# Optimization experiments

Hardware: AMD Instinct MI355X
Metric: run time of the kernel (lower is better)

## Reference

```python
import jax, jax.numpy as jnp
import numpy as np
from jax import lax

EPS = 1e-8

def squash(x, axis=-1):
    # s = (|x|^2 / (1+|x|^2)) * x / |x|, norm over `axis`
    sq = jnp.sum(x * x, axis=axis, keepdims=True)
    return (sq / (1.0 + sq)) * x / jnp.sqrt(sq + EPS)

def _conv(x, w, b, stride):
    y = lax.conv_general_dilated(x, w, window_strides=(stride, stride), padding='VALID',
                                 dimension_numbers=('NCHW', 'OIHW', 'NCHW'))
    return y + b[None, :, None, None]

def setup_inputs() -> dict:
    key = jax.random.key(0)
    ks = jax.random.split(key, 12)
    B = 256
    return {
        'x': jax.random.uniform(ks[0], (B, 1, 28, 28), jnp.float32),
        'conv1_w': jax.random.normal(ks[1], (256, 1, 9, 9), jnp.float32) * 0.1,
        'conv1_b': jax.random.normal(ks[2], (256,), jnp.float32) * 0.01,
        'conv2_w': jax.random.normal(ks[3], (256, 256, 9, 9), jnp.float32) * 0.02,
        'conv2_b': jax.random.normal(ks[4], (256,), jnp.float32) * 0.01,
        'W': jax.random.normal(ks[5], (10, 1152, 8, 16), jnp.float32) * 0.05,
        'dec_w1': jax.random.normal(ks[6], (160, 512), jnp.float32) * 0.05,
        'dec_b1': jnp.zeros((512,), jnp.float32),
        'dec_w2': jax.random.normal(ks[7], (512, 1024), jnp.float32) * 0.04,
        'dec_b2': jnp.zeros((1024,), jnp.float32),
        'dec_w3': jax.random.normal(ks[8], (1024, 784), jnp.float32) * 0.03,
        'dec_b3': jnp.zeros((784,), jnp.float32),
    }

def reference(x, conv1_w, conv1_b, conv2_w, conv2_b, W, dec_w1, dec_b1, dec_w2, dec_b2, dec_w3, dec_b3):
    B = x.shape[0]
    h = jax.nn.relu(_conv(x, conv1_w, conv1_b, 1))          # [B,256,20,20]
    h = jax.nn.relu(_conv(h, conv2_w, conv2_b, 2))          # [B,256,6,6]
    u = squash(h.reshape(B, 1152, 8))                       # [B,1152,8]
    # u_hat[b,c,n,f] = sum_d u[b,n,d] * W[c,n,d,f]
    u_hat = jnp.einsum('bnd,cndf->bcnf', u, W)              # [B,10,1152,16]
    # dynamic routing, 3 iterations; softmax over the 1152 input-capsule axis
    # (faithful to original: softmax dim=2, b constant along the 16 axis)
    b_logits = jnp.zeros((B, 10, 1152), u_hat.dtype)
    v = None
    for i in range(3):
        c = jax.nn.softmax(b_logits, axis=2)                # [B,10,1152]
        s = jnp.einsum('bcn,bcnf->bcf', c, u_hat)           # [B,10,16]
        v = squash(s)
        if i != 2:
            b_logits = b_logits + jnp.einsum('bcf,bcnf->bcn', v, u_hat)
    class_probs = jnp.sqrt(jnp.sum(v * v, axis=-1) + EPS)   # [B,10]
    idx = jnp.argmax(class_probs, axis=-1)
    mask = jax.nn.one_hot(idx, 10, dtype=v.dtype)           # [B,10]
    r = (v * mask[:, :, None]).reshape(B, 160)
    r = jax.nn.relu(r @ dec_w1 + dec_b1)
    r = jax.nn.relu(r @ dec_w2 + dec_b2)
    recons = jax.nn.sigmoid(r @ dec_w3 + dec_b3)            # [B,784]
    return (class_probs, recons)
```

## Files before the change

### kernel.cpp

```cpp
#include <hip/hip_runtime.h>
#include <hip/hip_bf16.h>
#include <math.h>

typedef _Float16 f16;
typedef f16 f16x8 __attribute__((ext_vector_type(8)));
typedef f16 f16x4 __attribute__((ext_vector_type(4)));
typedef float f32x16 __attribute__((ext_vector_type(16)));


__global__ __launch_bounds__(256) void conv1_kernel(
    const float* __restrict__ x, const float* __restrict__ w,
    const float* __restrict__ bias, f16* __restrict__ outh,
    float* __restrict__ outf, int mode)
{
    const int b = blockIdx.y;
    const int cg = blockIdx.x;
    const int t = threadIdx.x;

    __shared__ float xs[784];
    __shared__ float wt[81 * 16];
    __shared__ float bs[16];

    for (int i = t; i < 784; i += 256) xs[i] = x[b * 784 + i];
    for (int i = t; i < 1296; i += 256) {
        int k = i >> 4, cc = i & 15;
        wt[i] = w[(cg * 16 + cc) * 81 + k];
    }
    if (t < 16) bs[t] = bias[cg * 16 + t];
    __syncthreads();

    if (t >= 200) return;
    const int pos = t * 2;
    const int oy = pos / 20, ox = pos % 20;
    float4 A0[4], A1[4];
    #pragma unroll
    for (int g = 0; g < 4; ++g) { A0[g] = make_float4(0,0,0,0); A1[g] = make_float4(0,0,0,0); }

    for (int ky = 0; ky < 9; ++ky) {
        const float* xr = &xs[(oy + ky) * 28 + ox];
        #pragma unroll
        for (int kx = 0; kx < 9; ++kx) {
            float x0 = xr[kx], x1 = xr[kx + 1];
            const float4* wp = (const float4*)&wt[(ky * 9 + kx) << 4];
            #pragma unroll
            for (int g = 0; g < 4; ++g) {
                float4 wv = wp[g];
                A0[g].x = fmaf(x0, wv.x, A0[g].x); A0[g].y = fmaf(x0, wv.y, A0[g].y);
                A0[g].z = fmaf(x0, wv.z, A0[g].z); A0[g].w = fmaf(x0, wv.w, A0[g].w);
                A1[g].x = fmaf(x1, wv.x, A1[g].x); A1[g].y = fmaf(x1, wv.y, A1[g].y);
                A1[g].z = fmaf(x1, wv.z, A1[g].z); A1[g].w = fmaf(x1, wv.w, A1[g].w);
            }
        }
    }

    float va[16], vb[16];
    #pragma unroll
    for (int g = 0; g < 4; ++g) {
        va[g*4+0] = fmaxf(A0[g].x + bs[g*4+0], 0.f);
        va[g*4+1] = fmaxf(A0[g].y + bs[g*4+1], 0.f);
        va[g*4+2] = fmaxf(A0[g].z + bs[g*4+2], 0.f);
        va[g*4+3] = fmaxf(A0[g].w + bs[g*4+3], 0.f);
        vb[g*4+0] = fmaxf(A1[g].x + bs[g*4+0], 0.f);
        vb[g*4+1] = fmaxf(A1[g].y + bs[g*4+1], 0.f);
        vb[g*4+2] = fmaxf(A1[g].z + bs[g*4+2], 0.f);
        vb[g*4+3] = fmaxf(A1[g].w + bs[g*4+3], 0.f);
    }

    if (mode == 0) {
        size_t base0 = ((size_t)b * 400 + pos) * 256 + cg * 16;
        f16x8 H;
        #pragma unroll
        for (int q = 0; q < 8; ++q) H[q] = (f16)va[q];
        *(f16x8*)(outh + base0) = H;
        #pragma unroll
        for (int q = 0; q < 8; ++q) H[q] = (f16)va[8+q];
        *(f16x8*)(outh + base0 + 8) = H;
        size_t base1 = base0 + 256;
        #pragma unroll
        for (int q = 0; q < 8; ++q) H[q] = (f16)vb[q];
        *(f16x8*)(outh + base1) = H;
        #pragma unroll
        for (int q = 0; q < 8; ++q) H[q] = (f16)vb[8+q];
        *(f16x8*)(outh + base1 + 8) = H;
    } else {
        #pragma unroll
        for (int q = 0; q < 16; ++q) {
            size_t base = (size_t)(b * 256 + cg * 16 + q) * 400 + pos;
            outf[base] = va[q]; outf[base + 1] = vb[q];
        }
    }
}

__global__ __launch_bounds__(256) void wprep_kernel(
    const float* __restrict__ w, f16* __restrict__ Wf,
    const float* __restrict__ W, f16* __restrict__ Wr)
{
    const int co = blockIdx.x, t = threadIdx.x;
    __shared__ float wl[20736];
    for (int i = t; i < 20736; i += 256) wl[i] = w[(size_t)co * 20736 + i];
    __syncthreads();
    for (int tap = 0; tap < 81; ++tap) {
        size_t o = ((size_t)tap * 256 + co) * 256 + t;
        Wf[o] = (f16)wl[t * 81 + tap];
    }
    const int base = co * 5760;
    for (int i = t; i < 5760; i += 256) Wr[base + i] = (f16)W[base + i];
}


#define GLOAD16(GSRC, LDST) \
    __builtin_amdgcn_global_load_lds( \
        (const __attribute__((address_space(1))) void*)(GSRC), \
        (__attribute__((address_space(3))) void*)(LDST), 16, 0, 0)

__global__ __launch_bounds__(256, 2) void conv2_async(
    const f16* __restrict__ A, const f16* __restrict__ B,
    float* __restrict__ partial, int nslice, int spk, int nwg)
{
    const int cpx = nwg >> 3;
    const int wg = (blockIdx.x & 7) * cpx + (blockIdx.x >> 3);
    const int mblk = wg / nslice;
    const int kslice = wg % nslice;

    const int t = threadIdx.x;
    const int lane = t & 63, w = t >> 6;
    const int wm = w >> 1, wn = w & 1;

    __shared__ f16 sA3[3][4096];
    __shared__ f16 sB3[3][8192];

    const f16* aBase[2];
    #pragma unroll
    for (int q = 0; q < 2; ++q) {
        int m = mblk * 128 + q * 64 + lane;
        int b_ = m / 36, s_ = m % 36;
        aBase[q] = A + b_ * 102400 + ((s_ / 6) * 40 + (s_ % 6) * 2) * 256 + w * 8;
    }
    const f16* bBase[4];
    #pragma unroll
    for (int q = 0; q < 4; ++q)
        bBase[q] = B + (q * 64 + lane) * 256 + w * 8;

    const int g0 = kslice * spk;
    const int len = min(spk, 648 - g0);

    auto issue = [&](int gstep, int buf) {
        const int tap = gstep >> 3;
        const int kc = (gstep & 7) << 5;
        const int ky = tap / 9, kx = tap - ky * 9;
        const int ao = (ky * 20 + kx) * 256 + kc;
        const int bo = tap * 65536 + kc;
        f16* la = &sA3[buf][w * 1024];
        f16* lb = &sB3[buf][w * 2048];
        GLOAD16(aBase[0] + ao, la);
        GLOAD16(aBase[1] + ao, la + 512);
        GLOAD16(bBase[0] + bo, lb);
        GLOAD16(bBase[1] + bo, lb + 512);
        GLOAD16(bBase[2] + bo, lb + 1024);
        GLOAD16(bBase[3] + bo, lb + 1536);
    };

    const int kh = lane >> 5;
    const int rArow = wm * 64 + (lane & 31);
    const int rBrow = wn * 128 + (lane & 31);
    int offA[2], offB[2];
    #pragma unroll
    for (int h = 0; h < 2; ++h) {
        offA[h] = ((h * 2 + kh) << 11) + rArow * 16;
        offB[h] = ((h * 2 + kh) << 12) + rBrow * 16;
    }

    f32x16 acc00 = {}, acc01 = {}, acc02 = {}, acc03 = {};
    f32x16 acc10 = {}, acc11 = {}, acc12 = {}, acc13 = {};

    issue(g0, 0);
    if (len > 1) issue(g0 + 1, 1);

    for (int s = 0; s < len; ++s) {
        const int buf = s % 3;
        if (s + 1 < len) { asm volatile("s_waitcnt vmcnt(6)" ::: "memory"); }
        else             { asm volatile("s_waitcnt vmcnt(0)" ::: "memory"); }
        __builtin_amdgcn_s_barrier();
        asm volatile("" ::: "memory");
        if (s + 2 < len) issue(g0 + s + 2, (s + 2) % 3);

        const char* baseA = (const char*)sA3 + buf * 8192;
        const char* baseB = (const char*)sB3 + buf * 16384;
        #pragma unroll
        for (int h = 0; h < 2; ++h) {
            f16x8 a0 = *(const f16x8*)(baseA + offA[h]);
            f16x8 a1 = *(const f16x8*)(baseA + offA[h] + 512);
            f16x8 b0 = *(const f16x8*)(baseB + offB[h]);
            f16x8 b1 = *(const f16x8*)(baseB + offB[h] + 512);
            f16x8 b2 = *(const f16x8*)(baseB + offB[h] + 1024);
            f16x8 b3 = *(const f16x8*)(baseB + offB[h] + 1536);
            acc00 = __builtin_amdgcn_mfma_f32_32x32x16_f16(a0, b0, acc00, 0, 0, 0);
            acc01 = __builtin_amdgcn_mfma_f32_32x32x16_f16(a0, b1, acc01, 0, 0, 0);
            acc02 = __builtin_amdgcn_mfma_f32_32x32x16_f16(a0, b2, acc02, 0, 0, 0);
            acc03 = __builtin_amdgcn_mfma_f32_32x32x16_f16(a0, b3, acc03, 0, 0, 0);
            acc10 = __builtin_amdgcn_mfma_f32_32x32x16_f16(a1, b0, acc10, 0, 0, 0);
            acc11 = __builtin_amdgcn_mfma_f32_32x32x16_f16(a1, b1, acc11, 0, 0, 0);
            acc12 = __builtin_amdgcn_mfma_f32_32x32x16_f16(a1, b2, acc12, 0, 0, 0);
            acc13 = __builtin_amdgcn_mfma_f32_32x32x16_f16(a1, b3, acc13, 0, 0, 0);
        }
    }

    float* pp = partial + (size_t)kslice * 2359296;
    const int colb = wn * 128 + (lane & 31);
    const int rowb = mblk * 128 + wm * 64 + 4 * (lane >> 5);
    #pragma unroll
    for (int a = 0; a < 2; ++a) {
        #pragma unroll
        for (int nf = 0; nf < 4; ++nf) {
            const f32x16 v = (a == 0)
                ? (nf == 0 ? acc00 : nf == 1 ? acc01 : nf == 2 ? acc02 : acc03)
                : (nf == 0 ? acc10 : nf == 1 ? acc11 : nf == 2 ? acc12 : acc13);
            const int col = colb + nf * 32;
            const int rb = rowb + a * 32;
            #pragma unroll
            for (int r = 0; r < 16; ++r) {
                int row = rb + (r & 3) + 8 * (r >> 2);
                pp[(size_t)row * 256 + col] = v[r];
            }
        }
    }
}

__global__ __launch_bounds__(256) void reduce_kernel(
    const float* __restrict__ partial, const float* __restrict__ bias,
    float* __restrict__ u, int ks)
{
    const int b = blockIdx.x, t = threadIdx.x;
    __shared__ float ld[36 * 260];
    const int cog = t & 63;
    const int srow = t >> 6;
    const float4 bv = *(const float4*)(bias + cog * 4);
    #pragma unroll
    for (int q = 0; q < 9; ++q) {
        const int s = srow + q * 4;
        const size_t idx = ((size_t)(b * 36 + s)) * 256 + cog * 4;
        float a0 = bv.x, a1 = bv.y, a2 = bv.z, a3 = bv.w;
        for (int k = 0; k < ks; ++k) {
            float4 p = *(const float4*)(partial + (size_t)k * 2359296 + idx);
            a0 += p.x; a1 += p.y; a2 += p.z; a3 += p.w;
        }
        float4 a = make_float4(fmaxf(a0, 0.f), fmaxf(a1, 0.f),
                               fmaxf(a2, 0.f), fmaxf(a3, 0.f));
        *(float4*)&ld[s * 260 + cog * 4] = a;
    }
    __syncthreads();
    for (int n = t; n < 1152; n += 256) {
        const int f0 = n * 8;
        float vals[8]; float sq = 0.f;
        int co = f0 / 36;
        int si = f0 - co * 36;
        #pragma unroll
        for (int d = 0; d < 8; ++d) {
            float v = ld[si * 260 + co];
            vals[d] = v; sq += v * v;
            if (++si == 36) { si = 0; ++co; }
        }
        float scale = (sq / (1.f + sq)) / sqrtf(sq + 1e-8f);
        #pragma unroll
        for (int d = 0; d < 8; ++d) u[(size_t)b * 9216 + f0 + d] = vals[d] * scale;
    }
}

#define C2_CHUNK 2
__global__ __launch_bounds__(384) void conv2_kernel(
    const float* __restrict__ in, const float* __restrict__ w,
    const float* __restrict__ bias, float* __restrict__ out)
{
    const int bg = blockIdx.y;
    const int ct = blockIdx.x;
    const int t = threadIdx.x;

    __shared__ float wl[C2_CHUNK][81][64];
    __shared__ float il[C2_CHUNK][4][20][24];

    const int cg = t & 15;
    const int slot = t >> 4;
    const int bb = slot / 6;
    const int oy = slot % 6;

    float4 acc[6];
    #pragma unroll
    for (int i = 0; i < 6; ++i) acc[i] = make_float4(0,0,0,0);

    for (int cc0 = 0; cc0 < 256; cc0 += C2_CHUNK) {
        for (int idx = t; idx < C2_CHUNK * 5184; idx += 384) {
            int ci = idx / 5184;
            int r = idx - ci * 5184;
            int kk = r >> 6;
            int co = r & 63;
            wl[ci][kk][co] = w[(size_t)(ct * 64 + co) * 20736 + (cc0 + ci) * 81 + kk];
        }
        for (int idx = t; idx < C2_CHUNK * 1600; idx += 384) {
            int ci = idx / 1600;
            int r = idx - ci * 1600;
            int bb2 = r / 400;
            int p = r - bb2 * 400;
            int y = p / 20;
            int xx = p - y * 20;
            il[ci][bb2][y][(xx & 1) * 12 + (xx >> 1)] =
                in[(size_t)((bg * 4 + bb2) * 256 + cc0 + ci) * 400 + p];
        }
        __syncthreads();

        #pragma unroll
        for (int ci = 0; ci < C2_CHUNK; ++ci) {
            for (int ky = 0; ky < 9; ++ky) {
                const int y = oy * 2 + ky;
                const float4* rowp = (const float4*)&il[ci][bb][y][0];
                float a[24];
                #pragma unroll
                for (int q = 0; q < 6; ++q) *(((float4*)a) + q) = rowp[q];
                #pragma unroll
                for (int kx = 0; kx < 9; ++kx) {
                    const int k = ky * 9 + kx;
                    float4 wv = *(const float4*)&wl[ci][k][cg * 4];
                    const int base = (kx & 1) ? (12 + (kx >> 1)) : (kx >> 1);
                    #pragma unroll
                    for (int ox = 0; ox < 6; ++ox) {
                        float av = a[base + ox];
                        acc[ox].x = fmaf(av, wv.x, acc[ox].x);
                        acc[ox].y = fmaf(av, wv.y, acc[ox].y);
                        acc[ox].z = fmaf(av, wv.z, acc[ox].z);
                        acc[ox].w = fmaf(av, wv.w, acc[ox].w);
                    }
                }
            }
        }
        __syncthreads();
    }

    const int b = bg * 4 + bb;
    const int c0 = ct * 64 + cg * 4;
    float4 bv = *(const float4*)&bias[c0];
    #pragma unroll
    for (int ox = 0; ox < 6; ++ox) {
        int sdx = oy * 6 + ox;
        size_t ob = (size_t)b * 9216 + sdx;
        out[ob + (size_t)(c0 + 0) * 36] = fmaxf(acc[ox].x + bv.x, 0.f);
        out[ob + (size_t)(c0 + 1) * 36] = fmaxf(acc[ox].y + bv.y, 0.f);
        out[ob + (size_t)(c0 + 2) * 36] = fmaxf(acc[ox].z + bv.z, 0.f);
        out[ob + (size_t)(c0 + 3) * 36] = fmaxf(acc[ox].w + bv.w, 0.f);
    }
}

__global__ __launch_bounds__(256) void squash_kernel(float* __restrict__ h)
{
    const int cap = blockIdx.x * 256 + threadIdx.x;
    float4* p = (float4*)(h + (size_t)cap * 8);
    float4 v0 = p[0], v1 = p[1];
    float sq = v0.x*v0.x + v0.y*v0.y + v0.z*v0.z + v0.w*v0.w
             + v1.x*v1.x + v1.y*v1.y + v1.z*v1.z + v1.w*v1.w;
    float scale = (sq / (1.f + sq)) / sqrtf(sq + 1e-8f);
    v0.x *= scale; v0.y *= scale; v0.z *= scale; v0.w *= scale;
    v1.x *= scale; v1.y *= scale; v1.z *= scale; v1.w *= scale;
    p[0] = v0; p[1] = v1;
}

__global__ __launch_bounds__(256) void routing_kernel(
    const float* __restrict__ u, const f16* __restrict__ Wr,
    float* __restrict__ cp_out, float* __restrict__ vbuf)
{
    const int wg = ((blockIdx.x & 7) * 320) + (blockIdx.x >> 3);
    const int c = wg >> 8;
    const int b = wg & 255;
    const int t = threadIdx.x;
    const int lane = t & 63, wid = t >> 6;

    __shared__ float uh[1152 * 16];
    __shared__ float cl[1152];
    __shared__ float red[256];
    __shared__ float rtmp[8];
    __shared__ float vv[16];

    {
        const int fg = t & 3, ng = t >> 2;
        const f16* Wc = Wr + (size_t)c * 147456;
        const float* ub = u + (size_t)b * 9216;
        for (int j = 0; j < 18; ++j) {
            int n = ng + (j << 6);
            const f16* wn = Wc + n * 128 + fg * 4;
            float4 u0 = *(const float4*)(ub + n * 8);
            float4 u1 = *(const float4*)(ub + n * 8 + 4);
            float ud[8] = {u0.x, u0.y, u0.z, u0.w, u1.x, u1.y, u1.z, u1.w};
            float ax = 0.f, ay = 0.f, az = 0.f, aw = 0.f;
            #pragma unroll
            for (int d = 0; d < 8; ++d) {
                f16x4 w4 = *(const f16x4*)(wn + (d << 4));
                ax = fmaf(ud[d], (float)w4[0], ax);
                ay = fmaf(ud[d], (float)w4[1], ay);
                az = fmaf(ud[d], (float)w4[2], az);
                aw = fmaf(ud[d], (float)w4[3], aw);
            }
            *(float4*)&uh[(n << 4) + (fg << 2)] = make_float4(ax, ay, az, aw);
        }
    }
    __syncthreads();

    float blr[5] = {0.f, 0.f, 0.f, 0.f, 0.f};
    const int nown = (t < 128) ? 5 : 4;

    for (int it = 0; it < 3; ++it) {
        float m = -1e30f;
        #pragma unroll
        for (int k = 0; k < 5; ++k) if (k < nown) m = fmaxf(m, blr[k]);
        #pragma unroll
        for (int o = 32; o > 0; o >>= 1) m = fmaxf(m, __shfl_xor(m, o));
        if (lane == 0) rtmp[wid] = m;
        __syncthreads();
        m = fmaxf(fmaxf(rtmp[0], rtmp[1]), fmaxf(rtmp[2], rtmp[3]));

        float sum = 0.f;
        #pragma unroll
        for (int k = 0; k < 5; ++k) if (k < nown) {
            float e = __expf(blr[k] - m);
            cl[t + (k << 8)] = e;
            sum += e;
        }
        #pragma unroll
        for (int o = 32; o > 0; o >>= 1) sum += __shfl_xor(sum, o);
        if (lane == 0) rtmp[4 + wid] = sum;
        __syncthreads();
        float inv = 1.f / (rtmp[4] + rtmp[5] + rtmp[6] + rtmp[7]);

        const int f = t & 15, g = t >> 4;
        float sacc = 0.f;
        for (int n = g; n < 1152; n += 16)
            sacc = fmaf(cl[n], uh[(n << 4) + f], sacc);
        red[(g << 4) + f] = sacc;
        __syncthreads();
        if (t < 16) {
            float sv = 0.f;
            #pragma unroll
            for (int gg = 0; gg < 16; ++gg) sv += red[(gg << 4) + t];
            sv *= inv;
            float sq = sv * sv;
            #pragma unroll
            for (int o = 8; o > 0; o >>= 1) sq += __shfl_xor(sq, o);
            float scale = (sq / (1.f + sq)) / sqrtf(sq + 1e-8f);
            vv[t] = sv * scale;
        }
        __syncthreads();

        if (it < 2) {
            #pragma unroll
            for (int k = 0; k < 5; ++k) if (k < nown) {
                const int n = t + (k << 8);
                const float4* up = (const float4*)&uh[n << 4];
                float4 q0 = up[0], q1 = up[1], q2 = up[2], q3 = up[3];
                blr[k] +=
                    q0.x*vv[0]  + q0.y*vv[1]  + q0.z*vv[2]  + q0.w*vv[3] +
                    q1.x*vv[4]  + q1.y*vv[5]  + q1.z*vv[6]  + q1.w*vv[7] +
                    q2.x*vv[8]  + q2.y*vv[9]  + q2.z*vv[10] + q2.w*vv[11] +
                    q3.x*vv[12] + q3.y*vv[13] + q3.z*vv[14] + q3.w*vv[15];
            }
        }
    }

    if (t < 16) {
        float v_ = vv[t];
        float s2 = v_ * v_;
        #pragma unroll
        for (int o = 8; o > 0; o >>= 1) s2 += __shfl_xor(s2, o);
        if (t == 0) cp_out[b * 10 + c] = sqrtf(s2 + 1e-8f);
        vbuf[((b * 10 + c) << 4) + t] = v_;
    }
}

__global__ __launch_bounds__(256) void dec1_kernel(
    const float* __restrict__ cp, const float* __restrict__ vbuf,
    const float* __restrict__ W1, const float* __restrict__ B1,
    float* __restrict__ h1)
{
    const int b = blockIdx.x, t = threadIdx.x;
    __shared__ float r16[16];

    float best = cp[b * 10];
    int idx = 0;
    #pragma unroll
    for (int cc = 1; cc < 10; ++cc) {
        float p = cp[b * 10 + cc];
        if (p > best) { best = p; idx = cc; }
    }
    if (t < 16) r16[t] = vbuf[(b * 10 + idx) * 16 + t];
    __syncthreads();

    float a0 = B1[t], a1 = B1[t + 256];
    const float* w = W1 + (size_t)idx * 16 * 512 + t;
    #pragma unroll
    for (int k = 0; k < 16; ++k) {
        float rv = r16[k];
        a0 = fmaf(rv, w[k * 512], a0);
        a1 = fmaf(rv, w[k * 512 + 256], a1);
    }
    h1[(size_t)b * 512 + t] = fmaxf(a0, 0.f);
    h1[(size_t)b * 512 + t + 256] = fmaxf(a1, 0.f);
}

__global__ __launch_bounds__(256) void dec2_kernel(
    const float* __restrict__ h1, const float* __restrict__ W2,
    const float* __restrict__ B2, float* __restrict__ h2)
{
    const int ot = blockIdx.x, bt = blockIdx.y, t = threadIdx.x;
    const int bb = bt * 16 + (t >> 4);
    const int o = ot * 128 + (t & 15) * 8;

    float acc[8];
    float4 bv0 = *(const float4*)(B2 + o);
    float4 bv1 = *(const float4*)(B2 + o + 4);
    acc[0]=bv0.x; acc[1]=bv0.y; acc[2]=bv0.z; acc[3]=bv0.w;
    acc[4]=bv1.x; acc[5]=bv1.y; acc[6]=bv1.z; acc[7]=bv1.w;

    const float* hr = h1 + (size_t)bb * 512;
    #pragma unroll 4
    for (int k = 0; k < 512; ++k) {
        float hv = hr[k];
        float4 w0 = *(const float4*)(W2 + (size_t)k * 1024 + o);
        float4 w1 = *(const float4*)(W2 + (size_t)k * 1024 + o + 4);
        acc[0] = fmaf(hv, w0.x, acc[0]); acc[1] = fmaf(hv, w0.y, acc[1]);
        acc[2] = fmaf(hv, w0.z, acc[2]); acc[3] = fmaf(hv, w0.w, acc[3]);
        acc[4] = fmaf(hv, w1.x, acc[4]); acc[5] = fmaf(hv, w1.y, acc[5]);
        acc[6] = fmaf(hv, w1.z, acc[6]); acc[7] = fmaf(hv, w1.w, acc[7]);
    }
    float* hw = h2 + (size_t)bb * 1024 + o;
    #pragma unroll
    for (int q = 0; q < 8; ++q) hw[q] = fmaxf(acc[q], 0.f);
}

__global__ __launch_bounds__(256) void dec3_kernel(
    const float* __restrict__ h2, const float* __restrict__ W3,
    const float* __restrict__ B3, float* __restrict__ out)
{
    const int ot = blockIdx.x, bt = blockIdx.y, t = threadIdx.x;
    const int bb = bt * 16 + (t >> 4);
    const int o = ot * 64 + (t & 15) * 4;
    if (o >= 784) return;

    float4 bv = *(const float4*)(B3 + o);
    float acc[4] = {bv.x, bv.y, bv.z, bv.w};

    const float* hr = h2 + (size_t)bb * 1024;
    #pragma unroll 4
    for (int k = 0; k < 1024; ++k) {
        float hv = hr[k];
        float4 w0 = *(const float4*)(W3 + (size_t)k * 784 + o);
        acc[0] = fmaf(hv, w0.x, acc[0]); acc[1] = fmaf(hv, w0.y, acc[1]);
        acc[2] = fmaf(hv, w0.z, acc[2]); acc[3] = fmaf(hv, w0.w, acc[3]);
    }
    float* ow = out + (size_t)bb * 784 + o;
    #pragma unroll
    for (int q = 0; q < 4; ++q) ow[q] = 1.f / (1.f + expf(-acc[q]));
}

extern "C" void kernel_launch(void* const* d_in, const int* in_sizes, int n_in,
                              void* d_out, int out_size, void* d_ws, size_t ws_size,
                              hipStream_t stream) {
    const float* x   = (const float*)d_in[0];
    const float* w1  = (const float*)d_in[1];
    const float* b1  = (const float*)d_in[2];
    const float* w2  = (const float*)d_in[3];
    const float* b2  = (const float*)d_in[4];
    const float* W   = (const float*)d_in[5];
    const float* dw1 = (const float*)d_in[6];
    const float* db1 = (const float*)d_in[7];
    const float* dw2 = (const float*)d_in[8];
    const float* db2 = (const float*)d_in[9];
    const float* dw3 = (const float*)d_in[10];
    const float* db3 = (const float*)d_in[11];

    float* ws   = (float*)d_ws;
    float* outp = (float*)d_out;

    const size_t avail = ws_size / 4;
    int ks = 0;
    if      (avail >= 16498688ull + 7*2359296ull + 40960ull) ks = 7;
    else if (avail >= 16498688ull + 6*2359296ull + 40960ull) ks = 6;
    else if (avail >= 16498688ull + 4*2359296ull + 40960ull) ks = 4;
    else if (avail >= 16498688ull + 2*2359296ull + 40960ull) ks = 2;
    else if (avail >= 16498688ull + 1*2359296ull + 40960ull) ks = 1;

    if (ks > 0) {
        f16* Af = (f16*)ws;
        f16* Wf = (f16*)(ws + 13107200);
        f16* Wr = (f16*)(ws + 15761408);
        float* partial = ws + 16498688;
        float* vbuf = ws + 16498688 + (size_t)ks * 2359296;
        float* u  = ws;
        float* h1 = ws + 13107200;
        float* h2 = ws + 13238272;

        const int nwg = 72 * ks;
        const int spk = (648 + ks - 1) / ks;
        conv1_kernel<<<dim3(16, 256), 256, 0, stream>>>(x, w1, b1, Af, nullptr, 0);
        wprep_kernel<<<256, 256, 0, stream>>>(w2, Wf, W, Wr);
        conv2_async<<<nwg, 256, 0, stream>>>(Af, Wf, partial, ks, spk, nwg);
        reduce_kernel<<<256, 256, 0, stream>>>(partial, b2, u, ks);
        routing_kernel<<<2560, 256, 0, stream>>>(u, Wr, outp, vbuf);
        dec1_kernel<<<256, 256, 0, stream>>>(outp, vbuf, dw1, db1, h1);
        dec2_kernel<<<dim3(8, 16), 256, 0, stream>>>(h1, dw2, db2, h2);
        dec3_kernel<<<dim3(13, 16), 256, 0, stream>>>(h2, dw3, db3, outp + 2560);
    } else {
        float* c1   = ws;
        float* c2   = c1 + 26214400;
        float* vbuf = c2 + 2359296;
        float* h1   = vbuf + 40960;
        float* h2   = h1 + 131072;
        f16* Wr     = (f16*)(h2 + 262144);
        conv1_kernel<<<dim3(16, 256), 256, 0, stream>>>(x, w1, b1, nullptr, c1, 1);
        wprep_kernel<<<256, 256, 0, stream>>>(w2, (f16*)(h2 + 262144 + 368640), W, Wr);
        conv2_kernel<<<dim3(4, 64), 384, 0, stream>>>(c1, w2, b2, c2);
        squash_kernel<<<1152, 256, 0, stream>>>(c2);
        routing_kernel<<<2560, 256, 0, stream>>>(c2, Wr, outp, vbuf);
        dec1_kernel<<<256, 256, 0, stream>>>(outp, vbuf, dw1, db1, h1);
        dec2_kernel<<<dim3(8, 16), 256, 0, stream>>>(h1, dw2, db2, h2);
        dec3_kernel<<<dim3(13, 16), 256, 0, stream>>>(h2, dw3, db3, outp + 2560);
    }
}
```

Baseline: 519.5 us.

## Process two batch items per routing workgroup with fp16 LDS storage

The routing kernel now handles two batch samples per workgroup, so each loaded W element is reused for two u_hat computations and the grid drops from 2560 to 1280 blocks. u_hat and the softmax coefficients are stored in LDS as fp16, which keeps the doubled working set at about the old LDS footprint. This roughly halves W global traffic and per-block overhead. The cost is fp16 rounding of u_hat and the coefficients, fewer blocks for latency hiding, and more registers per thread.

```diff
diff --git a/kernel.cpp b/kernel.cpp
--- a/kernel.cpp
+++ b/kernel.cpp
@@ -106,7 +106,6 @@
     const int base = co * 5760;
     for (int i = t; i < 5760; i += 256) Wr[base + i] = (f16)W[base + i];
 }
-
 
 #define GLOAD16(GSRC, LDST) \
     __builtin_amdgcn_global_load_lds( \
@@ -365,109 +364,150 @@
     const float* __restrict__ u, const f16* __restrict__ Wr,
     float* __restrict__ cp_out, float* __restrict__ vbuf)
 {
-    const int wg = ((blockIdx.x & 7) * 320) + (blockIdx.x >> 3);
-    const int c = wg >> 8;
-    const int b = wg & 255;
+    const int wg = ((blockIdx.x & 7) * 160) + (blockIdx.x >> 3);
+    const int c = wg >> 7;
+    const int bp = wg & 127;
+    const int b0 = bp * 2, b1 = b0 + 1;
     const int t = threadIdx.x;
     const int lane = t & 63, wid = t >> 6;
 
-    __shared__ float uh[1152 * 16];
-    __shared__ float cl[1152];
-    __shared__ float red[256];
-    __shared__ float rtmp[8];
-    __shared__ float vv[16];
+    __shared__ f16 uhh[2 * 1152 * 16];
+    __shared__ f16 clh[2 * 1152];
+    __shared__ float red[512];
+    __shared__ float rtmp[16];
+    __shared__ float vv[2][16];
 
     {
-        const int fg = t & 3, ng = t >> 2;
+        const int fg = t & 1;
+        const int ng = t >> 1;
         const f16* Wc = Wr + (size_t)c * 147456;
-        const float* ub = u + (size_t)b * 9216;
-        for (int j = 0; j < 18; ++j) {
-            int n = ng + (j << 6);
-            const f16* wn = Wc + n * 128 + fg * 4;
-            float4 u0 = *(const float4*)(ub + n * 8);
-            float4 u1 = *(const float4*)(ub + n * 8 + 4);
-            float ud[8] = {u0.x, u0.y, u0.z, u0.w, u1.x, u1.y, u1.z, u1.w};
-            float ax = 0.f, ay = 0.f, az = 0.f, aw = 0.f;
+        const float* ub0 = u + (size_t)b0 * 9216;
+        const float* ub1 = u + (size_t)b1 * 9216;
+        for (int j = 0; j < 9; ++j) {
+            const int n = ng + (j << 7);
+            const f16* wn = Wc + n * 128 + fg * 8;
+            float4 u00 = *(const float4*)(ub0 + n * 8);
+            float4 u01 = *(const float4*)(ub0 + n * 8 + 4);
+            float4 u10 = *(const float4*)(ub1 + n * 8);
+            float4 u11 = *(const float4*)(ub1 + n * 8 + 4);
+            float ud0[8] = {u00.x,u00.y,u00.z,u00.w,u01.x,u01.y,u01.z,u01.w};
+            float ud1[8] = {u10.x,u10.y,u10.z,u10.w,u11.x,u11.y,u11.z,u11.w};
+            float a0[8] = {0,0,0,0,0,0,0,0}, a1[8] = {0,0,0,0,0,0,0,0};
             #pragma unroll
             for (int d = 0; d < 8; ++d) {
-                f16x4 w4 = *(const f16x4*)(wn + (d << 4));
-                ax = fmaf(ud[d], (float)w4[0], ax);
-                ay = fmaf(ud[d], (float)w4[1], ay);
-                az = fmaf(ud[d], (float)w4[2], az);
-                aw = fmaf(ud[d], (float)w4[3], aw);
+                f16x8 w8 = *(const f16x8*)(wn + (d << 4));
+                #pragma unroll
+                for (int e = 0; e < 8; ++e) {
+                    float wf = (float)w8[e];
+                    a0[e] = fmaf(ud0[d], wf, a0[e]);
+                    a1[e] = fmaf(ud1[d], wf, a1[e]);
+                }
             }
-            *(float4*)&uh[(n << 4) + (fg << 2)] = make_float4(ax, ay, az, aw);
+            f16x8 h0, h1;
+            #pragma unroll
+            for (int e = 0; e < 8; ++e) { h0[e] = (f16)a0[e]; h1[e] = (f16)a1[e]; }
+            *(f16x8*)&uhh[(n << 4) + (fg << 3)] = h0;
+            *(f16x8*)&uhh[18432 + (n << 4) + (fg << 3)] = h1;
         }
     }
     __syncthreads();
 
-    float blr[5] = {0.f, 0.f, 0.f, 0.f, 0.f};
+    float blr0[5] = {0,0,0,0,0}, blr1[5] = {0,0,0,0,0};
     const int nown = (t < 128) ? 5 : 4;
 
     for (int it = 0; it < 3; ++it) {
-        float m = -1e30f;
-        #pragma unroll
-        for (int k = 0; k < 5; ++k) if (k < nown) m = fmaxf(m, blr[k]);
-        #pragma unroll
-        for (int o = 32; o > 0; o >>= 1) m = fmaxf(m, __shfl_xor(m, o));
-        if (lane == 0) rtmp[wid] = m;
+        float m0 = -1e30f, m1 = -1e30f;
+        #pragma unroll
+        for (int k = 0; k < 5; ++k) if (k < nown) {
+            m0 = fmaxf(m0, blr0[k]); m1 = fmaxf(m1, blr1[k]);
+        }
+        #pragma unroll
+        for (int o = 32; o > 0; o >>= 1) {
+            m0 = fmaxf(m0, __shfl_xor(m0, o));
+            m1 = fmaxf(m1, __shfl_xor(m1, o));
+        }
+        if (lane == 0) { rtmp[wid] = m0; rtmp[4 + wid] = m1; }
         __syncthreads();
-        m = fmaxf(fmaxf(rtmp[0], rtmp[1]), fmaxf(rtmp[2], rtmp[3]));
-
-        float sum = 0.f;
+        m0 = fmaxf(fmaxf(rtmp[0], rtmp[1]), fmaxf(rtmp[2], rtmp[3]));
+        m1 = fmaxf(fmaxf(rtmp[4], rtmp[5]), fmaxf(rtmp[6], rtmp[7]));
+
+        float s0 = 0.f, s1 = 0.f;
         #pragma unroll
         for (int k = 0; k < 5; ++k) if (k < nown) {
-            float e = __expf(blr[k] - m);
-            cl[t + (k << 8)] = e;
-            sum += e;
-        }
-        #pragma unroll
-        for (int o = 32; o > 0; o >>= 1) sum += __shfl_xor(sum, o);
-        if (lane == 0) rtmp[4 + wid] = sum;
+            float e0 = __expf(blr0[k] - m0);
+            float e1 = __expf(blr1[k] - m1);
+            clh[t + (k << 8)] = (f16)e0;
+            clh[1152 + t + (k << 8)] = (f16)e1;
+            s0 += e0; s1 += e1;
+        }
+        #pragma unroll
+        for (int o = 32; o > 0; o >>= 1) {
+            s0 += __shfl_xor(s0, o);
+            s1 += __shfl_xor(s1, o);
+        }
+        if (lane == 0) { rtmp[8 + wid] = s0; rtmp[12 + wid] = s1; }
         __syncthreads();
-        float inv = 1.f / (rtmp[4] + rtmp[5] + rtmp[6] + rtmp[7]);
+        const float inv0 = 1.f / (rtmp[8] + rtmp[9] + rtmp[10] + rtmp[11]);
+        const float inv1 = 1.f / (rtmp[12] + rtmp[13] + rtmp[14] + rtmp[15]);
 
         const int f = t & 15, g = t >> 4;
-        float sacc = 0.f;
-        for (int n = g; n < 1152; n += 16)
-            sacc = fmaf(cl[n], uh[(n << 4) + f], sacc);
-        red[(g << 4) + f] = sacc;
+        float sa0 = 0.f, sa1 = 0.f;
+        for (int n = g; n < 1152; n += 16) {
+            sa0 = fmaf((float)clh[n], (float)uhh[(n << 4) + f], sa0);
+            sa1 = fmaf((float)clh[1152 + n], (float)uhh[18432 + (n << 4) + f], sa1);
+        }
+        red[(g << 4) + f] = sa0;
+        red[256 + (g << 4) + f] = sa1;
         __syncthreads();
-        if (t < 16) {
+        if (t < 32) {
+            const int s = t >> 4;
+            const int ff = t & 15;
             float sv = 0.f;
             #pragma unroll
-            for (int gg = 0; gg < 16; ++gg) sv += red[(gg << 4) + t];
-            sv *= inv;
+            for (int gg = 0; gg < 16; ++gg) sv += red[s * 256 + (gg << 4) + ff];
+            sv *= (s == 0) ? inv0 : inv1;
             float sq = sv * sv;
             #pragma unroll
             for (int o = 8; o > 0; o >>= 1) sq += __shfl_xor(sq, o);
             float scale = (sq / (1.f + sq)) / sqrtf(sq + 1e-8f);
-            vv[t] = sv * scale;
+            vv[s][ff] = sv * scale;
         }
         __syncthreads();
 
         if (it < 2) {
+            float v0[16], v1[16];
+            #pragma unroll
+            for (int e = 0; e < 16; ++e) { v0[e] = vv[0][e]; v1[e] = vv[1][e]; }
             #pragma unroll
             for (int k = 0; k < 5; ++k) if (k < nown) {
                 const int n = t + (k << 8);
-                const float4* up = (const float4*)&uh[n << 4];
-                float4 q0 = up[0], q1 = up[1], q2 = up[2], q3 = up[3];
-                blr[k] +=
-                    q0.x*vv[0]  + q0.y*vv[1]  + q0.z*vv[2]  + q0.w*vv[3] +
-                    q1.x*vv[4]  + q1.y*vv[5]  + q1.z*vv[6]  + q1.w*vv[7] +
-                    q2.x*vv[8]  + q2.y*vv[9]  + q2.z*vv[10] + q2.w*vv[11] +
-                    q3.x*vv[12] + q3.y*vv[13] + q3.z*vv[14] + q3.w*vv[15];
+                f16x8 q0 = *(const f16x8*)&uhh[n << 4];
+                f16x8 q1 = *(const f16x8*)&uhh[(n << 4) + 8];
+                f16x8 r0 = *(const f16x8*)&uhh[18432 + (n << 4)];
+                f16x8 r1 = *(const f16x8*)&uhh[18432 + (n << 4) + 8];
+                float d0 = 0.f, d1 = 0.f;
+                #pragma unroll
+                for (int e = 0; e < 8; ++e) {
+                    d0 = fmaf((float)q0[e], v0[e], d0);
+                    d0 = fmaf((float)q1[e], v0[8 + e], d0);
+                    d1 = fmaf((float)r0[e], v1[e], d1);
+                    d1 = fmaf((float)r1[e], v1[8 + e], d1);
+                }
+                blr0[k] += d0; blr1[k] += d1;
             }
         }
     }
 
-    if (t < 16) {
-        float v_ = vv[t];
+    if (t < 32) {
+        const int s = t >> 4;
+        const int ff = t & 15;
+        float v_ = vv[s][ff];
         float s2 = v_ * v_;
         #pragma unroll
         for (int o = 8; o > 0; o >>= 1) s2 += __shfl_xor(s2, o);
-        if (t == 0) cp_out[b * 10 + c] = sqrtf(s2 + 1e-8f);
-        vbuf[((b * 10 + c) << 4) + t] = v_;
+        const int b = (s == 0) ? b0 : b1;
+        if (ff == 0) cp_out[b * 10 + c] = sqrtf(s2 + 1e-8f);
+        vbuf[((b * 10 + c) << 4) + ff] = v_;
     }
 }
 
@@ -599,7 +639,7 @@
         wprep_kernel<<<256, 256, 0, stream>>>(w2, Wf, W, Wr);
         conv2_async<<<nwg, 256, 0, stream>>>(Af, Wf, partial, ks, spk, nwg);
         reduce_kernel<<<256, 256, 0, stream>>>(partial, b2, u, ks);
-        routing_kernel<<<2560, 256, 0, stream>>>(u, Wr, outp, vbuf);
+        routing_kernel<<<1280, 256, 0, stream>>>(u, Wr, outp, vbuf);
         dec1_kernel<<<256, 256, 0, stream>>>(outp, vbuf, dw1, db1, h1);
         dec2_kernel<<<dim3(8, 16), 256, 0, stream>>>(h1, dw2, db2, h2);
         dec3_kernel<<<dim3(13, 16), 256, 0, stream>>>(h2, dw3, db3, outp + 2560);
@@ -614,7 +654,7 @@
         wprep_kernel<<<256, 256, 0, stream>>>(w2, (f16*)(h2 + 262144 + 368640), W, Wr);
         conv2_kernel<<<dim3(4, 64), 384, 0, stream>>>(c1, w2, b2, c2);
         squash_kernel<<<1152, 256, 0, stream>>>(c2);
-        routing_kernel<<<2560, 256, 0, stream>>>(c2, Wr, outp, vbuf);
+        routing_kernel<<<1280, 256, 0, stream>>>(c2, Wr, outp, vbuf);
         dec1_kernel<<<256, 256, 0, stream>>>(outp, vbuf, dw1, db1, h1);
         dec2_kernel<<<dim3(8, 16), 256, 0, stream>>>(h1, dw2, db2, h2);
         dec3_kernel<<<dim3(13, 16), 256, 0, stream>>>(h2, dw3, db3, outp + 2560);
```

Result: faster. 448.3 us (-13.7%).
